# Performance work log

Measured on AMD Instinct MI355X. Metric: run time of the kernel, lower is better.

## Reference

```python
import jax, jax.numpy as jnp
import numpy as np

EXPERT_CAPACITY = 320
RMS_EPS = 1e-6


def setup_inputs() -> dict:
    key = jax.random.key(0)
    k1, k2, k3, k4 = jax.random.split(key, 4)
    B, S, D, E, F = 8, 2048, 1024, 8, 2048
    data = jax.random.normal(k1, (B, S, D), dtype=jnp.float32)
    gate_w = jax.random.normal(k2, (D, E), dtype=jnp.float32) * 0.02
    w1 = jax.random.normal(k3, (E, D, F), dtype=jnp.float32) * 0.02
    w2 = jax.random.normal(k4, (E, F, D), dtype=jnp.float32) * 0.02
    rms_w = jnp.ones((D,), dtype=jnp.float32)
    return {"data": data, "gate_w": gate_w, "w1": w1, "w2": w2, "rms_w": rms_w}


def reference(data, gate_w, w1, w2, rms_w):
    B, S, D = data.shape
    E = gate_w.shape[1]
    C = EXPERT_CAPACITY

    # norm_fn: RMSNorm
    var = jnp.mean(data * data, axis=-1, keepdims=True)
    norm = data * jax.lax.rsqrt(var + RMS_EPS) * rms_w  # [B,S,D]

    # route (fp32 gate, no jitter)
    logits = jnp.einsum('bsd,de->bse', norm, gate_w)  # [B,S,E]
    probs = jax.nn.softmax(logits, axis=-1)
    eidx = jnp.argmax(probs, axis=-1)  # [B,S] top-1 expert
    onehot = jax.nn.one_hot(eidx, E, dtype=jnp.int32)  # [B,S,E]
    priority = jnp.cumsum(onehot, axis=1)  # position within expert per batch row
    mask = onehot * (priority <= C)  # capacity-masked dispatch mask [B,S,E]

    pos = jnp.take_along_axis(priority, eidx[..., None], axis=2)[..., 0] - 1  # [B,S]
    kept = jnp.take_along_axis(mask, eidx[..., None], axis=2)[..., 0].astype(bool)
    pos_oob = jnp.where(kept, pos, C)  # OOB -> dropped on scatter

    # dispatch: scatter kept tokens into [B,E,C,D] buffers
    b_idx = jnp.arange(B)[:, None]  # broadcast over S
    buf = jnp.zeros((B, E, C, D), dtype=norm.dtype)
    buf = buf.at[b_idx, eidx, pos_oob].set(norm, mode='drop')

    # per-expert FFN with gelu_new (tanh approx)
    h = jax.nn.gelu(jnp.einsum('becd,edf->becf', buf, w1), approximate=True)
    out_buf = jnp.einsum('becf,efd->becd', h, w2)  # [B,E,C,D]

    # combine: gather expert output; dropped tokens keep norm_data (clone semantics)
    pos_c = jnp.clip(pos_oob, 0, C - 1)
    y = out_buf[b_idx, eidx, pos_c]  # [B,S,D]
    next_states = jnp.where(kept[..., None], y, norm)

    max_prob = jnp.max(probs, axis=-1, keepdims=True)
    hidden = max_prob * next_states
    final = data + hidden  # dropout rate 0

    expert_index_out = jnp.argmax(mask, axis=-1)  # matches torch argmax over masked one-hot
    return final, logits, expert_index_out
```

## Files before the change

### kernel.cpp

```cpp
#include <hip/hip_runtime.h>

typedef __attribute__((ext_vector_type(8))) __bf16 bf16x8;
typedef __attribute__((ext_vector_type(4))) float f32x4;

#define DEVI __device__ __forceinline__

DEVI unsigned short f2bf(float f) {
    unsigned u = __builtin_bit_cast(unsigned, f);
    u += 0x7fffu + ((u >> 16) & 1u);
    return (unsigned short)(u >> 16);
}
DEVI float bf2f(unsigned short h) {
    unsigned u = ((unsigned)h) << 16;
    return __builtin_bit_cast(float, u);
}
DEVI float gelu_tanh(float x) {
    float u = 0.7978845608028654f * (x + 0.044715f * x * x * x);
    float t = 1.0f - 2.0f / (1.0f + __expf(2.0f * u));
    return 0.5f * x * (1.0f + t);
}
DEVI void gload16(const void* g, void* l) {
    __builtin_amdgcn_global_load_lds((const __attribute__((address_space(1))) unsigned int*)g,
                                     (__attribute__((address_space(3))) unsigned int*)l,
                                     16, 0, 0);
}

#define BB 8
#define SS 2048
#define DD 1024
#define EE 8
#define FF 2048
#define CC 320
#define NTOK (BB * SS)
#define MPE (BB * CC)
#define NSLOT (EE * MPE)

__global__ __launch_bounds__(256) void k_rms_gate(
    const float* __restrict__ data, const float* __restrict__ gate_w,
    const float* __restrict__ rms_w, unsigned short* __restrict__ norm_bf,
    float* __restrict__ logits_out, float* __restrict__ maxprob, int* __restrict__ eidx_out,
    float* __restrict__ outF)
{
    const int token = blockIdx.x;
    const int t = threadIdx.x;
    const float4 v = ((const float4*)(data + (size_t)token * DD))[t];
    float ss = v.x * v.x + v.y * v.y + v.z * v.z + v.w * v.w;
#pragma unroll
    for (int o = 32; o; o >>= 1) ss += __shfl_down(ss, o, 64);
    __shared__ float sred[4];
    __shared__ float slog[8];
    __shared__ float sacc[4][8];
    __shared__ float smp;
    if ((t & 63) == 0) sred[t >> 6] = ss;
    __syncthreads();
    const float tot = sred[0] + sred[1] + sred[2] + sred[3];
    const float scale = rsqrtf(tot * (1.0f / 1024.0f) + 1e-6f);
    const float4 w = ((const float4*)rms_w)[t];
    float nn[4] = { v.x * scale * w.x, v.y * scale * w.y, v.z * scale * w.z, v.w * scale * w.w };
    ushort4 nb;
    nb.x = f2bf(nn[0]); nb.y = f2bf(nn[1]); nb.z = f2bf(nn[2]); nb.w = f2bf(nn[3]);
    ((ushort4*)(norm_bf + (size_t)token * DD))[t] = nb;

    float acc[8] = {0, 0, 0, 0, 0, 0, 0, 0};
    const float4* g = (const float4*)(gate_w + t * 32);
#pragma unroll
    for (int d = 0; d < 4; ++d) {
        float4 p = g[2 * d], q = g[2 * d + 1];
        acc[0] += nn[d] * p.x; acc[1] += nn[d] * p.y; acc[2] += nn[d] * p.z; acc[3] += nn[d] * p.w;
        acc[4] += nn[d] * q.x; acc[5] += nn[d] * q.y; acc[6] += nn[d] * q.z; acc[7] += nn[d] * q.w;
    }
#pragma unroll
    for (int e = 0; e < 8; ++e) {
#pragma unroll
        for (int o = 32; o; o >>= 1) acc[e] += __shfl_down(acc[e], o, 64);
    }
    if ((t & 63) == 0) {
#pragma unroll
        for (int e = 0; e < 8; ++e) sacc[t >> 6][e] = acc[e];
    }
    __syncthreads();
    if (t < 8) {
        float l = sacc[0][t] + sacc[1][t] + sacc[2][t] + sacc[3][t];
        logits_out[(size_t)token * 8 + t] = l;
        slog[t] = l;
    }
    __syncthreads();
    if (t == 0) {
        float m = slog[0]; int am = 0;
#pragma unroll
        for (int e = 1; e < 8; ++e) { if (slog[e] > m) { m = slog[e]; am = e; } }
        float s = 0.f;
#pragma unroll
        for (int e = 0; e < 8; ++e) s += __expf(slog[e] - m);
        const float mp = 1.0f / s;
        maxprob[token] = mp;
        smp = mp;
        eidx_out[token] = am;
    }
    __syncthreads();
    const float mp = smp;
    float4 o;
    o.x = v.x + mp * nn[0]; o.y = v.y + mp * nn[1];
    o.z = v.z + mp * nn[2]; o.w = v.w + mp * nn[3];
    ((float4*)(outF + (size_t)token * DD))[t] = o;
}

__global__ __launch_bounds__(256) void k_route(
    const int* __restrict__ eidx, float* __restrict__ idxf_out,
    int* __restrict__ slot_token, int* __restrict__ zp)
{
    const int b = blockIdx.x, t = threadIdx.x;
    if (b == 0) { zp[t] = 0; zp[t + 256] = 0; zp[t + 512] = 0; zp[t + 768] = 0; }
    for (int i = t; i < EE * CC; i += 256) {
        int e = i / CC, c = i % CC;
        slot_token[e * MPE + b * CC + c] = -1;
    }
    const int base = b * SS + t * 8;
    int e8[8];
#pragma unroll
    for (int j = 0; j < 8; ++j) e8[j] = eidx[base + j];
    int cnt[8] = {0, 0, 0, 0, 0, 0, 0, 0};
#pragma unroll
    for (int j = 0; j < 8; ++j) {
#pragma unroll
        for (int q = 0; q < 8; ++q) cnt[q] += (e8[j] == q);
    }
    __shared__ int sc[8][256];
#pragma unroll
    for (int q = 0; q < 8; ++q) sc[q][t] = cnt[q];
    __syncthreads();
    for (int off = 1; off < 256; off <<= 1) {
        int v[8];
#pragma unroll
        for (int q = 0; q < 8; ++q) v[q] = (t >= off) ? sc[q][t - off] : 0;
        __syncthreads();
#pragma unroll
        for (int q = 0; q < 8; ++q) sc[q][t] += v[q];
        __syncthreads();
    }
    int run[8];
#pragma unroll
    for (int q = 0; q < 8; ++q) run[q] = (t == 0) ? 0 : sc[q][t - 1];
#pragma unroll
    for (int j = 0; j < 8; ++j) {
        const int e = e8[j];
        const int tok = base + j;
        int pos = 0;
#pragma unroll
        for (int q = 0; q < 8; ++q) if (q == e) { pos = run[q]; run[q]++; }
        const bool kept = pos < CC;
        idxf_out[tok] = (float)(kept ? e : 0);
        if (kept) slot_token[e * MPE + b * CC + pos] = tok;
    }
}

__global__ __launch_bounds__(256) void k_transcvt3(
    const float* __restrict__ w1, const float* __restrict__ w2,
    unsigned short* __restrict__ w1T, unsigned short* __restrict__ w2T)
{
    __shared__ float tile[64][68];
    const int bid = blockIdx.x, t = threadIdx.x;
    const float* src; unsigned short* dst; int C, R, tr, tc;
    if (bid < 4096) {
        const int e = bid >> 9, rem = bid & 511;
        tr = rem >> 5; tc = rem & 31;
        src = w1 + (size_t)e * (DD * FF); dst = w1T + (size_t)e * (DD * FF);
        R = DD; C = FF;
    } else {
        const int b2 = bid - 4096;
        const int e = b2 >> 9, rem = b2 & 511;
        tr = rem >> 4; tc = rem & 15;
        src = w2 + (size_t)e * (DD * FF); dst = w2T + (size_t)e * (DD * FF);
        R = FF; C = DD;
    }
    const int r = t >> 2, c0 = (t & 3) << 4;
    const float4* sp = (const float4*)(src + (size_t)(tr * 64 + r) * C + tc * 64 + c0);
#pragma unroll
    for (int i = 0; i < 4; ++i) *(float4*)&tile[r][c0 + 4 * i] = sp[i];
    __syncthreads();
    const int oc = t >> 2, i0 = (t & 3) << 4;
    union { unsigned short us[16]; int4 q[2]; } u;
#pragma unroll
    for (int i = 0; i < 16; ++i) u.us[i] = f2bf(tile[i0 + i][oc]);
    unsigned short* dp = dst + (size_t)(tc * 64 + oc) * R + tr * 64 + i0;
    *(int4*)dp = u.q[0];
    *(int4*)(dp + 8) = u.q[1];
}

#define LD_A(buf, h) { _Pragma("unroll") for (int mp_ = 0; mp_ < 4; ++mp_) { \
    const int lr_ = mp_ * 16 + rr; \
    _Pragma("unroll") for (int ks_ = 0; ks_ < 2; ++ks_) \
      ar_[mp_][ks_] = *(const bf16x8*)(sm + (buf) * 65536 + (h) * 16384 + wm * 8192 + lr_ * 128 + ((ks_ * 64 + g * 16) ^ (((lr_ >> 2) & 1) << 5))); } }

#define LD_B(buf, h, reg) { _Pragma("unroll") for (int np_ = 0; np_ < 2; ++np_) { \
    const int lr_ = np_ * 16 + rr; \
    _Pragma("unroll") for (int ks_ = 0; ks_ < 2; ++ks_) \
      reg[np_][ks_] = *(const bf16x8*)(sm + (buf) * 65536 + 32768 + (h) * 16384 + wn * 4096 + lr_ * 128 + ((ks_ * 64 + g * 16) ^ (((lr_ >> 2) & 1) << 5))); } }

#define MM(qa, qb, reg) { _Pragma("unroll") for (int ks_ = 0; ks_ < 2; ++ks_) \
    _Pragma("unroll") for (int mp_ = 0; mp_ < 4; ++mp_) \
    _Pragma("unroll") for (int np_ = 0; np_ < 2; ++np_) \
      acc[(qa) * 4 + mp_][(qb) * 2 + np_] = __builtin_amdgcn_mfma_f32_16x16x32_bf16(ar_[mp_][ks_], reg[np_][ks_], acc[(qa) * 4 + mp_][(qb) * 2 + np_], 0, 0, 0); }

#define ST_A(buf, h, kt) { \
    gload16(srcA[h][0] + (kt) * 64, sm + (buf) * 65536 + (h) * 16384 + tid * 16); \
    gload16(srcA[h][1] + (kt) * 64, sm + (buf) * 65536 + (h) * 16384 + 8192 + tid * 16); }
#define ST_B(buf, h, kt) { \
    gload16(srcB[h][0] + (kt) * 64, sm + (buf) * 65536 + 32768 + (h) * 16384 + tid * 16); \
    gload16(srcB[h][1] + (kt) * 64, sm + (buf) * 65536 + 32768 + (h) * 16384 + 8192 + tid * 16); }

#define PH_TOP  __builtin_amdgcn_s_barrier(); \
                asm volatile("s_waitcnt lgkmcnt(0)" ::: "memory"); \
                __builtin_amdgcn_s_setprio(1)
#define PH_END  __builtin_amdgcn_s_setprio(0); __builtin_amdgcn_s_barrier()
#define PH_END_VM4 __builtin_amdgcn_s_setprio(0); \
                asm volatile("s_waitcnt vmcnt(4)" ::: "memory"); __builtin_amdgcn_s_barrier()
#define PH_END_VM0 __builtin_amdgcn_s_setprio(0); \
                asm volatile("s_waitcnt vmcnt(0)" ::: "memory"); __builtin_amdgcn_s_barrier()

template <int MODE, int K, int NT_N>
__global__ __launch_bounds__(512) void k_gemm8(
    const unsigned short* __restrict__ Ap, const unsigned short* __restrict__ Bt,
    unsigned short* __restrict__ H, const int* __restrict__ slot_token,
    const float* __restrict__ maxprob, const float* __restrict__ data,
    float* __restrict__ outF, const unsigned short* __restrict__ zp)
{
    __shared__ __align__(16) unsigned char sm[131072];
    const int bid = blockIdx.x;
    const int e = bid & 7;
    const int inner = bid >> 3;
    const int tm = inner / NT_N, tn = inner % NT_N;
    const int tid = threadIdx.x;
    const int L = tid & 63;
    const int wm = tid >> 8;
    const int wn = (tid >> 6) & 3;
    const int rr = L & 15, g = L >> 4;
    const int slot0 = e * MPE + tm * 256;
    const int N = NT_N * 256;

    const unsigned short* srcA[2][2];
    const unsigned short* srcB[2][2];
#pragma unroll
    for (int h = 0; h < 2; ++h)
#pragma unroll
      for (int p = 0; p < 2; ++p) {
        const int o = p * 8192 + tid * 16;
        const int lo = o ^ (((o >> 9) & 1) << 5);
        const int cb = lo & 127;
        const int arr = (lo >> 7) & 63;
        const int arow = p * 128 + h * 64 + arr;
        if (MODE == 0) {
            const int tok = slot_token[slot0 + arow];
            srcA[h][p] = (tok < 0 ? zp : Ap + (size_t)tok * (size_t)K) + (cb >> 1);
        } else {
            srcA[h][p] = Ap + (size_t)(slot0 + arow) * (size_t)K + (cb >> 1);
        }
        const int bwn = o >> 12;
        const int brr = (lo >> 7) & 31;
        const int nrow = tn * 256 + bwn * 64 + h * 32 + brr;
        srcB[h][p] = Bt + ((size_t)e * N + nrow) * (size_t)K + (cb >> 1);
    }

    f32x4 acc[8][4];
#pragma unroll
    for (int m = 0; m < 8; ++m)
#pragma unroll
      for (int n = 0; n < 4; ++n) acc[m][n] = 0.f;
    bf16x8 ar_[4][2], br0_[2][2], br1_[2][2];

    ST_A(0, 0, 0); ST_B(0, 0, 0); ST_A(0, 1, 0); ST_B(0, 1, 0);
    ST_A(1, 0, 1); ST_B(1, 1, 1);
    asm volatile("s_waitcnt vmcnt(4)" ::: "memory");
    __builtin_amdgcn_s_barrier();

    const int NT = K / 64;
    const int NITER = NT / 2;
    for (int it = 0; it < NITER - 1; ++it) {
        const int t1 = 2 * it + 1;
        LD_A(0, 0); LD_B(0, 0, br0_); ST_A(1, 1, t1);
        PH_TOP; MM(0, 0, br0_); PH_END;
        LD_B(0, 1, br1_); ST_B(1, 0, t1);
        PH_TOP; MM(0, 1, br1_); PH_END;
        LD_A(0, 1); ST_A(0, 0, t1 + 1);
        PH_TOP; MM(1, 1, br1_); PH_END;
        ST_B(0, 1, t1 + 1);
        PH_TOP; MM(1, 0, br0_); PH_END_VM4;
        LD_A(1, 0); LD_B(1, 0, br0_); ST_A(0, 1, t1 + 1);
        PH_TOP; MM(0, 0, br0_); PH_END;
        LD_B(1, 1, br1_); ST_B(0, 0, t1 + 1);
        PH_TOP; MM(0, 1, br1_); PH_END;
        LD_A(1, 1); ST_A(1, 0, t1 + 2);
        PH_TOP; MM(1, 1, br1_); PH_END;
        ST_B(1, 1, t1 + 2);
        PH_TOP; MM(1, 0, br0_); PH_END_VM4;
    }
    {
        LD_A(0, 0); LD_B(0, 0, br0_); ST_A(1, 1, NT - 1);
        PH_TOP; MM(0, 0, br0_); PH_END;
        LD_B(0, 1, br1_); ST_B(1, 0, NT - 1);
        PH_TOP; MM(0, 1, br1_); PH_END;
        LD_A(0, 1);
        PH_TOP; MM(1, 1, br1_); PH_END;
        PH_TOP; MM(1, 0, br0_); PH_END_VM0;
        LD_A(1, 0); LD_B(1, 0, br0_);
        PH_TOP; MM(0, 0, br0_); PH_END;
        LD_B(1, 1, br1_);
        PH_TOP; MM(0, 1, br1_); PH_END;
        LD_A(1, 1);
        PH_TOP; MM(1, 1, br1_); PH_END;
        PH_TOP; MM(1, 0, br0_); PH_END;
    }

    unsigned short* lo16 = (unsigned short*)sm;
#pragma unroll
    for (int hb = 0; hb < 2; ++hb) {
        if (wm == hb) {
#pragma unroll
            for (int m = 0; m < 8; ++m)
#pragma unroll
              for (int n = 0; n < 4; ++n) {
                f32x4 a = acc[m][n];
#pragma unroll
                for (int j = 0; j < 4; ++j) {
                    float x = a[j];
                    if (MODE == 0) x = gelu_tanh(x);
                    lo16[(m * 16 + g * 4 + j) * 260 + wn * 64 + n * 16 + rr] = f2bf(x);
                }
              }
        }
        __syncthreads();
#pragma unroll
        for (int rd = 0; rd < 8; ++rd) {
            const int idx = rd * 512 + tid;
            const int row = idx >> 5, c8 = (idx & 31) << 3;
            if (MODE == 0) {
                int4 v = *(const int4*)(lo16 + row * 260 + c8);
                *(int4*)(H + (size_t)(slot0 + hb * 128 + row) * FF + (size_t)tn * 256 + c8) = v;
            } else {
                const int tok = slot_token[slot0 + hb * 128 + row];
                if (tok >= 0) {
                    const float mp = maxprob[tok];
                    int4 yv = *(const int4*)(lo16 + row * 260 + c8);
                    const unsigned short* yy = (const unsigned short*)&yv;
                    const size_t go = (size_t)tok * DD + (size_t)tn * 256 + c8;
                    float4 d0 = *(const float4*)(data + go);
                    float4 d1 = *(const float4*)(data + go + 4);
                    float4 o0, o1;
                    o0.x = d0.x + mp * bf2f(yy[0]); o0.y = d0.y + mp * bf2f(yy[1]);
                    o0.z = d0.z + mp * bf2f(yy[2]); o0.w = d0.w + mp * bf2f(yy[3]);
                    o1.x = d1.x + mp * bf2f(yy[4]); o1.y = d1.y + mp * bf2f(yy[5]);
                    o1.z = d1.z + mp * bf2f(yy[6]); o1.w = d1.w + mp * bf2f(yy[7]);
                    *(float4*)(outF + go) = o0;
                    *(float4*)(outF + go + 4) = o1;
                }
            }
        }
        __syncthreads();
    }
}

extern "C" void kernel_launch(void* const* d_in, const int* in_sizes, int n_in,
                              void* d_out, int out_size, void* d_ws, size_t ws_size,
                              hipStream_t stream)
{
    (void)in_sizes; (void)n_in; (void)out_size; (void)ws_size;
    const float* data   = (const float*)d_in[0];
    const float* gate_w = (const float*)d_in[1];
    const float* w1     = (const float*)d_in[2];
    const float* w2     = (const float*)d_in[3];
    const float* rms_w  = (const float*)d_in[4];

    float* outF   = (float*)d_out;
    float* logits = outF + (size_t)NTOK * DD;
    float* idxf   = logits + (size_t)NTOK * EE;

    char* ws = (char*)d_ws;
    const size_t SZ_NORM = (size_t)NTOK * DD * 2;
    const size_t SZ_W1T  = (size_t)EE * DD * FF * 2;
    const size_t SZ_W2T  = SZ_W1T;
    const size_t SZ_H    = (size_t)NSLOT * FF * 2;
    unsigned short* norm_bf = (unsigned short*)(ws);
    unsigned short* w1T     = (unsigned short*)(ws + SZ_NORM);
    unsigned short* w2T     = (unsigned short*)(ws + SZ_NORM + SZ_W1T);
    unsigned short* Hbuf    = (unsigned short*)(ws + SZ_NORM + SZ_W1T + SZ_W2T);
    char* small             = ws + SZ_NORM + SZ_W1T + SZ_W2T + SZ_H;
    int*   slot_token = (int*)(small);
    int*   eidx       = (int*)(small + NSLOT * 4);
    float* maxprob    = (float*)(small + NSLOT * 4 + NTOK * 4);
    int*   zp         = (int*)(small + NSLOT * 4 + NTOK * 4 + NTOK * 4);

    k_rms_gate<<<NTOK, 256, 0, stream>>>(data, gate_w, rms_w, norm_bf, logits, maxprob, eidx, outF);
    k_route<<<BB, 256, 0, stream>>>(eidx, idxf, slot_token, zp);
    k_transcvt3<<<8192, 256, 0, stream>>>(w1, w2, w1T, w2T);
    k_gemm8<0, 1024, 8><<<640, 512, 0, stream>>>(norm_bf, w1T, Hbuf, slot_token,
                                                 nullptr, nullptr, nullptr, (const unsigned short*)zp);
    k_gemm8<1, 2048, 4><<<320, 512, 0, stream>>>(Hbuf, w2T, nullptr, slot_token,
                                                 maxprob, data, outF, nullptr);
}
```

Before: 565.4 us.

## Shrink expert GEMM tiles to 256x128 with new LDS swizzle and pipeline

```diff
diff --git a/kernel.cpp b/kernel.cpp
--- a/kernel.cpp
+++ b/kernel.cpp
@@ -187,128 +187,113 @@
     *(int4*)(dp + 8) = u.q[1];
 }
 
+#define AOFF(buf, h) ((buf) * 32768 + (h) * 16384)
+#define BOFF(buf, bh) (65536 + (buf) * 16384 + (bh) * 8192)
+
+#define ST_A(buf, h, kt) { \
+    gload16(srcA[h][0] + (kt) * 64, sm + AOFF(buf, h) + tid * 16); \
+    gload16(srcA[h][1] + (kt) * 64, sm + AOFF(buf, h) + 8192 + tid * 16); }
+#define ST_B(buf, bh, kt) { \
+    gload16(srcB[bh] + (kt) * 64, sm + BOFF(buf, bh) + tid * 16); }
+
 #define LD_A(buf, h) { _Pragma("unroll") for (int mp_ = 0; mp_ < 4; ++mp_) { \
-    const int lr_ = mp_ * 16 + rr; \
     _Pragma("unroll") for (int ks_ = 0; ks_ < 2; ++ks_) \
-      ar_[mp_][ks_] = *(const bf16x8*)(sm + (buf) * 65536 + (h) * 16384 + wm * 8192 + lr_ * 128 + ((ks_ * 64 + g * 16) ^ (((lr_ >> 2) & 1) << 5))); } }
-
-#define LD_B(buf, h, reg) { _Pragma("unroll") for (int np_ = 0; np_ < 2; ++np_) { \
-    const int lr_ = np_ * 16 + rr; \
+      ar_[mp_][ks_] = *(const bf16x8*)(sm + AOFF(buf, h) + wm * 8192 + (mp_ * 16 + rr) * 128 \
+                                       + ((ks_ * 64 + g * 16) ^ ((rr & 7) << 4))); } }
+#define LD_B(buf) { _Pragma("unroll") for (int qb_ = 0; qb_ < 2; ++qb_) { \
     _Pragma("unroll") for (int ks_ = 0; ks_ < 2; ++ks_) \
-      reg[np_][ks_] = *(const bf16x8*)(sm + (buf) * 65536 + 32768 + (h) * 16384 + wn * 4096 + lr_ * 128 + ((ks_ * 64 + g * 16) ^ (((lr_ >> 2) & 1) << 5))); } }
-
-#define MM(qa, qb, reg) { _Pragma("unroll") for (int ks_ = 0; ks_ < 2; ++ks_) \
+      br_[qb_][ks_] = *(const bf16x8*)(sm + BOFF(buf, qb_) + wn * 2048 + rr * 128 \
+                                       + ((ks_ * 64 + g * 16) ^ ((rr & 7) << 4))); } }
+
+#define MM(qa) { _Pragma("unroll") for (int ks_ = 0; ks_ < 2; ++ks_) \
     _Pragma("unroll") for (int mp_ = 0; mp_ < 4; ++mp_) \
-    _Pragma("unroll") for (int np_ = 0; np_ < 2; ++np_) \
-      acc[(qa) * 4 + mp_][(qb) * 2 + np_] = __builtin_amdgcn_mfma_f32_16x16x32_bf16(ar_[mp_][ks_], reg[np_][ks_], acc[(qa) * 4 + mp_][(qb) * 2 + np_], 0, 0, 0); }
-
-#define ST_A(buf, h, kt) { \
-    gload16(srcA[h][0] + (kt) * 64, sm + (buf) * 65536 + (h) * 16384 + tid * 16); \
-    gload16(srcA[h][1] + (kt) * 64, sm + (buf) * 65536 + (h) * 16384 + 8192 + tid * 16); }
-#define ST_B(buf, h, kt) { \
-    gload16(srcB[h][0] + (kt) * 64, sm + (buf) * 65536 + 32768 + (h) * 16384 + tid * 16); \
-    gload16(srcB[h][1] + (kt) * 64, sm + (buf) * 65536 + 32768 + (h) * 16384 + 8192 + tid * 16); }
+    _Pragma("unroll") for (int qb_ = 0; qb_ < 2; ++qb_) \
+      acc[(qa) * 4 + mp_][qb_] = __builtin_amdgcn_mfma_f32_16x16x32_bf16(ar_[mp_][ks_], br_[qb_][ks_], acc[(qa) * 4 + mp_][qb_], 0, 0, 0); }
 
 #define PH_TOP  __builtin_amdgcn_s_barrier(); \
                 asm volatile("s_waitcnt lgkmcnt(0)" ::: "memory"); \
                 __builtin_amdgcn_s_setprio(1)
 #define PH_END  __builtin_amdgcn_s_setprio(0); __builtin_amdgcn_s_barrier()
-#define PH_END_VM4 __builtin_amdgcn_s_setprio(0); \
-                asm volatile("s_waitcnt vmcnt(4)" ::: "memory"); __builtin_amdgcn_s_barrier()
+#define PH_END_VM3 __builtin_amdgcn_s_setprio(0); \
+                asm volatile("s_waitcnt vmcnt(3)" ::: "memory"); __builtin_amdgcn_s_barrier()
 #define PH_END_VM0 __builtin_amdgcn_s_setprio(0); \
                 asm volatile("s_waitcnt vmcnt(0)" ::: "memory"); __builtin_amdgcn_s_barrier()
 
-template <int MODE, int K, int NT_N>
-__global__ __launch_bounds__(512) void k_gemm8(
+template <int MODE, int K, int NN>
+__global__ __launch_bounds__(512) void k_gemm4(
     const unsigned short* __restrict__ Ap, const unsigned short* __restrict__ Bt,
     unsigned short* __restrict__ H, const int* __restrict__ slot_token,
     const float* __restrict__ maxprob, const float* __restrict__ data,
     float* __restrict__ outF, const unsigned short* __restrict__ zp)
 {
-    __shared__ __align__(16) unsigned char sm[131072];
+    __shared__ __align__(16) unsigned char sm[98304];
+    const int ntn = NN >> 7;
     const int bid = blockIdx.x;
     const int e = bid & 7;
     const int inner = bid >> 3;
-    const int tm = inner / NT_N, tn = inner % NT_N;
+    const int tm = inner / ntn, tn = inner % ntn;
     const int tid = threadIdx.x;
     const int L = tid & 63;
     const int wm = tid >> 8;
     const int wn = (tid >> 6) & 3;
     const int rr = L & 15, g = L >> 4;
     const int slot0 = e * MPE + tm * 256;
-    const int N = NT_N * 256;
 
     const unsigned short* srcA[2][2];
-    const unsigned short* srcB[2][2];
+    const unsigned short* srcB[2];
 #pragma unroll
     for (int h = 0; h < 2; ++h)
 #pragma unroll
       for (int p = 0; p < 2; ++p) {
         const int o = p * 8192 + tid * 16;
-        const int lo = o ^ (((o >> 9) & 1) << 5);
-        const int cb = lo & 127;
-        const int arr = (lo >> 7) & 63;
-        const int arow = p * 128 + h * 64 + arr;
+        const int cb = (o & 127) ^ (((o >> 7) & 7) << 4);
+        const int arow = p * 128 + h * 64 + ((o >> 7) & 63);
         if (MODE == 0) {
             const int tok = slot_token[slot0 + arow];
             srcA[h][p] = (tok < 0 ? zp : Ap + (size_t)tok * (size_t)K) + (cb >> 1);
         } else {
             srcA[h][p] = Ap + (size_t)(slot0 + arow) * (size_t)K + (cb >> 1);
         }
-        const int bwn = o >> 12;
-        const int brr = (lo >> 7) & 31;
-        const int nrow = tn * 256 + bwn * 64 + h * 32 + brr;
-        srcB[h][p] = Bt + ((size_t)e * N + nrow) * (size_t)K + (cb >> 1);
-    }
-
-    f32x4 acc[8][4];
-#pragma unroll
-    for (int m = 0; m < 8; ++m)
-#pragma unroll
-      for (int n = 0; n < 4; ++n) acc[m][n] = 0.f;
-    bf16x8 ar_[4][2], br0_[2][2], br1_[2][2];
-
-    ST_A(0, 0, 0); ST_B(0, 0, 0); ST_A(0, 1, 0); ST_B(0, 1, 0);
+      }
+#pragma unroll
+    for (int bh = 0; bh < 2; ++bh) {
+        const int o = tid * 16;
+        const int cb = (o & 127) ^ (((o >> 7) & 7) << 4);
+        const int nrow = tn * 128 + (o >> 11) * 32 + bh * 16 + ((o >> 7) & 15);
+        srcB[bh] = Bt + ((size_t)e * NN + nrow) * (size_t)K + (cb >> 1);
+    }
+
+    f32x4 acc[8][2];
+#pragma unroll
+    for (int m = 0; m < 8; ++m) { acc[m][0] = 0.f; acc[m][1] = 0.f; }
+    bf16x8 ar_[4][2], br_[2][2];
+
+    ST_A(0, 0, 0); ST_B(0, 1, 0); ST_A(0, 1, 0); ST_B(0, 0, 0);
     ST_A(1, 0, 1); ST_B(1, 1, 1);
-    asm volatile("s_waitcnt vmcnt(4)" ::: "memory");
+    asm volatile("s_waitcnt vmcnt(3)" ::: "memory");
     __builtin_amdgcn_s_barrier();
 
     const int NT = K / 64;
-    const int NITER = NT / 2;
-    for (int it = 0; it < NITER - 1; ++it) {
-        const int t1 = 2 * it + 1;
-        LD_A(0, 0); LD_B(0, 0, br0_); ST_A(1, 1, t1);
-        PH_TOP; MM(0, 0, br0_); PH_END;
-        LD_B(0, 1, br1_); ST_B(1, 0, t1);
-        PH_TOP; MM(0, 1, br1_); PH_END;
-        LD_A(0, 1); ST_A(0, 0, t1 + 1);
-        PH_TOP; MM(1, 1, br1_); PH_END;
-        ST_B(0, 1, t1 + 1);
-        PH_TOP; MM(1, 0, br0_); PH_END_VM4;
-        LD_A(1, 0); LD_B(1, 0, br0_); ST_A(0, 1, t1 + 1);
-        PH_TOP; MM(0, 0, br0_); PH_END;
-        LD_B(1, 1, br1_); ST_B(0, 0, t1 + 1);
-        PH_TOP; MM(0, 1, br1_); PH_END;
-        LD_A(1, 1); ST_A(1, 0, t1 + 2);
-        PH_TOP; MM(1, 1, br1_); PH_END;
-        ST_B(1, 1, t1 + 2);
-        PH_TOP; MM(1, 0, br0_); PH_END_VM4;
+    for (int it = 0; it < NT / 2 - 1; ++it) {
+        const int v = 2 * it + 1;
+        LD_A(0, 0); LD_B(0); ST_A(1, 1, v); ST_B(1, 0, v);
+        PH_TOP; MM(0); PH_END;
+        LD_A(0, 1); ST_A(0, 0, v + 1); ST_B(0, 1, v + 1);
+        PH_TOP; MM(1); PH_END_VM3;
+        LD_A(1, 0); LD_B(1); ST_A(0, 1, v + 1); ST_B(0, 0, v + 1);
+        PH_TOP; MM(0); PH_END;
+        LD_A(1, 1); ST_A(1, 0, v + 2); ST_B(1, 1, v + 2);
+        PH_TOP; MM(1); PH_END_VM3;
     }
     {
-        LD_A(0, 0); LD_B(0, 0, br0_); ST_A(1, 1, NT - 1);
-        PH_TOP; MM(0, 0, br0_); PH_END;
-        LD_B(0, 1, br1_); ST_B(1, 0, NT - 1);
-        PH_TOP; MM(0, 1, br1_); PH_END;
+        LD_A(0, 0); LD_B(0); ST_A(1, 1, NT - 1); ST_B(1, 0, NT - 1);
+        PH_TOP; MM(0); PH_END;
         LD_A(0, 1);
-        PH_TOP; MM(1, 1, br1_); PH_END;
-        PH_TOP; MM(1, 0, br0_); PH_END_VM0;
-        LD_A(1, 0); LD_B(1, 0, br0_);
-        PH_TOP; MM(0, 0, br0_); PH_END;
-        LD_B(1, 1, br1_);
-        PH_TOP; MM(0, 1, br1_); PH_END;
+        PH_TOP; MM(1); PH_END_VM0;
+        LD_A(1, 0); LD_B(1);
+        PH_TOP; MM(0); PH_END;
         LD_A(1, 1);
-        PH_TOP; MM(1, 1, br1_); PH_END;
-        PH_TOP; MM(1, 0, br0_); PH_END;
+        PH_TOP; MM(1); PH_END;
     }
 
     unsigned short* lo16 = (unsigned short*)sm;
@@ -318,31 +303,31 @@
 #pragma unroll
             for (int m = 0; m < 8; ++m)
 #pragma unroll
-              for (int n = 0; n < 4; ++n) {
-                f32x4 a = acc[m][n];
+              for (int qb = 0; qb < 2; ++qb) {
+                f32x4 a = acc[m][qb];
 #pragma unroll
                 for (int j = 0; j < 4; ++j) {
                     float x = a[j];
                     if (MODE == 0) x = gelu_tanh(x);
-                    lo16[(m * 16 + g * 4 + j) * 260 + wn * 64 + n * 16 + rr] = f2bf(x);
+                    lo16[(m * 16 + g * 4 + j) * 132 + wn * 32 + qb * 16 + rr] = f2bf(x);
                 }
               }
         }
         __syncthreads();
 #pragma unroll
-        for (int rd = 0; rd < 8; ++rd) {
+        for (int rd = 0; rd < 4; ++rd) {
             const int idx = rd * 512 + tid;
-            const int row = idx >> 5, c8 = (idx & 31) << 3;
+            const int row = idx >> 4, c8 = (idx & 15) << 3;
             if (MODE == 0) {
-                int4 v = *(const int4*)(lo16 + row * 260 + c8);
-                *(int4*)(H + (size_t)(slot0 + hb * 128 + row) * FF + (size_t)tn * 256 + c8) = v;
+                int4 v = *(const int4*)(lo16 + row * 132 + c8);
+                *(int4*)(H + (size_t)(slot0 + hb * 128 + row) * FF + (size_t)tn * 128 + c8) = v;
             } else {
                 const int tok = slot_token[slot0 + hb * 128 + row];
                 if (tok >= 0) {
                     const float mp = maxprob[tok];
-                    int4 yv = *(const int4*)(lo16 + row * 260 + c8);
+                    int4 yv = *(const int4*)(lo16 + row * 132 + c8);
                     const unsigned short* yy = (const unsigned short*)&yv;
-                    const size_t go = (size_t)tok * DD + (size_t)tn * 256 + c8;
+                    const size_t go = (size_t)tok * DD + (size_t)tn * 128 + c8;
                     float4 d0 = *(const float4*)(data + go);
                     float4 d1 = *(const float4*)(data + go + 4);
                     float4 o0, o1;
@@ -392,8 +377,8 @@
     k_rms_gate<<<NTOK, 256, 0, stream>>>(data, gate_w, rms_w, norm_bf, logits, maxprob, eidx, outF);
     k_route<<<BB, 256, 0, stream>>>(eidx, idxf, slot_token, zp);
     k_transcvt3<<<8192, 256, 0, stream>>>(w1, w2, w1T, w2T);
-    k_gemm8<0, 1024, 8><<<640, 512, 0, stream>>>(norm_bf, w1T, Hbuf, slot_token,
-                                                 nullptr, nullptr, nullptr, (const unsigned short*)zp);
-    k_gemm8<1, 2048, 4><<<320, 512, 0, stream>>>(Hbuf, w2T, nullptr, slot_token,
-                                                 maxprob, data, outF, nullptr);
-}
+    k_gemm4<0, 1024, 2048><<<1280, 512, 0, stream>>>(norm_bf, w1T, Hbuf, slot_token,
+                                                     nullptr, nullptr, nullptr, (const unsigned short*)zp);
+    k_gemm4<1, 2048, 1024><<<640, 512, 0, stream>>>(Hbuf, w2T, nullptr, slot_token,
+                                                    maxprob, data, outF, nullptr);
+}
```

Measured after the change: 531.3 us. 1.06x faster.

## Use one wave per token in RMS/gate and fix LDS swizzles

Applied to the files above, without the earlier changes.

```diff
diff --git a/kernel.cpp b/kernel.cpp
--- a/kernel.cpp
+++ b/kernel.cpp
@@ -41,68 +41,81 @@
     float* __restrict__ logits_out, float* __restrict__ maxprob, int* __restrict__ eidx_out,
     float* __restrict__ outF)
 {
-    const int token = blockIdx.x;
-    const int t = threadIdx.x;
-    const float4 v = ((const float4*)(data + (size_t)token * DD))[t];
-    float ss = v.x * v.x + v.y * v.y + v.z * v.z + v.w * v.w;
+    const int token = blockIdx.x * 4 + (threadIdx.x >> 6);
+    const int lane = threadIdx.x & 63;
+    const float* dp = data + (size_t)token * DD;
+
+    float4 v[4];
+#pragma unroll
+    for (int s = 0; s < 4; ++s) v[s] = *(const float4*)(dp + s * 256 + lane * 4);
+    float ss = 0.f;
+#pragma unroll
+    for (int s = 0; s < 4; ++s)
+        ss += v[s].x * v[s].x + v[s].y * v[s].y + v[s].z * v[s].z + v[s].w * v[s].w;
 #pragma unroll
     for (int o = 32; o; o >>= 1) ss += __shfl_down(ss, o, 64);
-    __shared__ float sred[4];
-    __shared__ float slog[8];
-    __shared__ float sacc[4][8];
-    __shared__ float smp;
-    if ((t & 63) == 0) sred[t >> 6] = ss;
-    __syncthreads();
-    const float tot = sred[0] + sred[1] + sred[2] + sred[3];
+    const float tot = __shfl(ss, 0, 64);
     const float scale = rsqrtf(tot * (1.0f / 1024.0f) + 1e-6f);
-    const float4 w = ((const float4*)rms_w)[t];
-    float nn[4] = { v.x * scale * w.x, v.y * scale * w.y, v.z * scale * w.z, v.w * scale * w.w };
-    ushort4 nb;
-    nb.x = f2bf(nn[0]); nb.y = f2bf(nn[1]); nb.z = f2bf(nn[2]); nb.w = f2bf(nn[3]);
-    ((ushort4*)(norm_bf + (size_t)token * DD))[t] = nb;
+
+    float nn[16];
+#pragma unroll
+    for (int s = 0; s < 4; ++s) {
+        const float4 w = *(const float4*)(rms_w + s * 256 + lane * 4);
+        nn[s * 4 + 0] = v[s].x * scale * w.x;
+        nn[s * 4 + 1] = v[s].y * scale * w.y;
+        nn[s * 4 + 2] = v[s].z * scale * w.z;
+        nn[s * 4 + 3] = v[s].w * scale * w.w;
+        ushort4 nb;
+        nb.x = f2bf(nn[s * 4 + 0]); nb.y = f2bf(nn[s * 4 + 1]);
+        nb.z = f2bf(nn[s * 4 + 2]); nb.w = f2bf(nn[s * 4 + 3]);
+        *(ushort4*)(norm_bf + (size_t)token * DD + s * 256 + lane * 4) = nb;
+    }
 
     float acc[8] = {0, 0, 0, 0, 0, 0, 0, 0};
-    const float4* g = (const float4*)(gate_w + t * 32);
-#pragma unroll
-    for (int d = 0; d < 4; ++d) {
-        float4 p = g[2 * d], q = g[2 * d + 1];
-        acc[0] += nn[d] * p.x; acc[1] += nn[d] * p.y; acc[2] += nn[d] * p.z; acc[3] += nn[d] * p.w;
-        acc[4] += nn[d] * q.x; acc[5] += nn[d] * q.y; acc[6] += nn[d] * q.z; acc[7] += nn[d] * q.w;
-    }
+#pragma unroll
+    for (int s = 0; s < 4; ++s)
+#pragma unroll
+      for (int j = 0; j < 4; ++j) {
+        const float4* g = (const float4*)(gate_w + (size_t)(s * 256 + lane * 4 + j) * 8);
+        const float4 p = g[0], q = g[1];
+        const float x = nn[s * 4 + j];
+        acc[0] += x * p.x; acc[1] += x * p.y; acc[2] += x * p.z; acc[3] += x * p.w;
+        acc[4] += x * q.x; acc[5] += x * q.y; acc[6] += x * q.z; acc[7] += x * q.w;
+      }
 #pragma unroll
     for (int e = 0; e < 8; ++e) {
 #pragma unroll
         for (int o = 32; o; o >>= 1) acc[e] += __shfl_down(acc[e], o, 64);
     }
-    if ((t & 63) == 0) {
-#pragma unroll
-        for (int e = 0; e < 8; ++e) sacc[t >> 6][e] = acc[e];
-    }
-    __syncthreads();
-    if (t < 8) {
-        float l = sacc[0][t] + sacc[1][t] + sacc[2][t] + sacc[3][t];
-        logits_out[(size_t)token * 8 + t] = l;
-        slog[t] = l;
-    }
-    __syncthreads();
-    if (t == 0) {
-        float m = slog[0]; int am = 0;
-#pragma unroll
-        for (int e = 1; e < 8; ++e) { if (slog[e] > m) { m = slog[e]; am = e; } }
+
+    float mp = 0.f;
+    if (lane == 0) {
+        float m = acc[0]; int am = 0;
+#pragma unroll
+        for (int e = 1; e < 8; ++e) { if (acc[e] > m) { m = acc[e]; am = e; } }
         float s = 0.f;
 #pragma unroll
-        for (int e = 0; e < 8; ++e) s += __expf(slog[e] - m);
-        const float mp = 1.0f / s;
+        for (int e = 0; e < 8; ++e) s += __expf(acc[e] - m);
+        mp = 1.0f / s;
         maxprob[token] = mp;
-        smp = mp;
         eidx_out[token] = am;
     }
-    __syncthreads();
-    const float mp = smp;
-    float4 o;
-    o.x = v.x + mp * nn[0]; o.y = v.y + mp * nn[1];
-    o.z = v.z + mp * nn[2]; o.w = v.w + mp * nn[3];
-    ((float4*)(outF + (size_t)token * DD))[t] = o;
+    mp = __shfl(mp, 0, 64);
+#pragma unroll
+    for (int e = 0; e < 8; ++e) {
+        const float l = __shfl(acc[e], 0, 64);
+        if (lane == e) logits_out[(size_t)token * 8 + e] = l;
+    }
+
+#pragma unroll
+    for (int s = 0; s < 4; ++s) {
+        float4 o;
+        o.x = v[s].x + mp * nn[s * 4 + 0];
+        o.y = v[s].y + mp * nn[s * 4 + 1];
+        o.z = v[s].z + mp * nn[s * 4 + 2];
+        o.w = v[s].w + mp * nn[s * 4 + 3];
+        *(float4*)(outF + (size_t)token * DD + s * 256 + lane * 4) = o;
+    }
 }
 
 __global__ __launch_bounds__(256) void k_route(
@@ -158,7 +171,7 @@
     const float* __restrict__ w1, const float* __restrict__ w2,
     unsigned short* __restrict__ w1T, unsigned short* __restrict__ w2T)
 {
-    __shared__ float tile[64][68];
+    __shared__ float tile[64][65];
     const int bid = blockIdx.x, t = threadIdx.x;
     const float* src; unsigned short* dst; int C, R, tr, tc;
     if (bid < 4096) {
@@ -190,12 +203,12 @@
 #define LD_A(buf, h) { _Pragma("unroll") for (int mp_ = 0; mp_ < 4; ++mp_) { \
     const int lr_ = mp_ * 16 + rr; \
     _Pragma("unroll") for (int ks_ = 0; ks_ < 2; ++ks_) \
-      ar_[mp_][ks_] = *(const bf16x8*)(sm + (buf) * 65536 + (h) * 16384 + wm * 8192 + lr_ * 128 + ((ks_ * 64 + g * 16) ^ (((lr_ >> 2) & 1) << 5))); } }
+      ar_[mp_][ks_] = *(const bf16x8*)(sm + (buf) * 65536 + (h) * 16384 + wm * 8192 + lr_ * 128 + ((ks_ * 64 + g * 16) ^ ((lr_ & 7) << 4))); } }
 
 #define LD_B(buf, h, reg) { _Pragma("unroll") for (int np_ = 0; np_ < 2; ++np_) { \
     const int lr_ = np_ * 16 + rr; \
     _Pragma("unroll") for (int ks_ = 0; ks_ < 2; ++ks_) \
-      reg[np_][ks_] = *(const bf16x8*)(sm + (buf) * 65536 + 32768 + (h) * 16384 + wn * 4096 + lr_ * 128 + ((ks_ * 64 + g * 16) ^ (((lr_ >> 2) & 1) << 5))); } }
+      reg[np_][ks_] = *(const bf16x8*)(sm + (buf) * 65536 + 32768 + (h) * 16384 + wn * 4096 + lr_ * 128 + ((ks_ * 64 + g * 16) ^ ((lr_ & 7) << 4))); } }
 
 #define MM(qa, qb, reg) { _Pragma("unroll") for (int ks_ = 0; ks_ < 2; ++ks_) \
     _Pragma("unroll") for (int mp_ = 0; mp_ < 4; ++mp_) \
@@ -245,9 +258,8 @@
 #pragma unroll
       for (int p = 0; p < 2; ++p) {
         const int o = p * 8192 + tid * 16;
-        const int lo = o ^ (((o >> 9) & 1) << 5);
-        const int cb = lo & 127;
-        const int arr = (lo >> 7) & 63;
+        const int cb = (o & 127) ^ (((o >> 7) & 7) << 4);
+        const int arr = (o >> 7) & 63;
         const int arow = p * 128 + h * 64 + arr;
         if (MODE == 0) {
             const int tok = slot_token[slot0 + arow];
@@ -256,7 +268,7 @@
             srcA[h][p] = Ap + (size_t)(slot0 + arow) * (size_t)K + (cb >> 1);
         }
         const int bwn = o >> 12;
-        const int brr = (lo >> 7) & 31;
+        const int brr = (o >> 7) & 31;
         const int nrow = tn * 256 + bwn * 64 + h * 32 + brr;
         srcB[h][p] = Bt + ((size_t)e * N + nrow) * (size_t)K + (cb >> 1);
     }
@@ -389,7 +401,7 @@
     float* maxprob    = (float*)(small + NSLOT * 4 + NTOK * 4);
     int*   zp         = (int*)(small + NSLOT * 4 + NTOK * 4 + NTOK * 4);
 
-    k_rms_gate<<<NTOK, 256, 0, stream>>>(data, gate_w, rms_w, norm_bf, logits, maxprob, eidx, outF);
+    k_rms_gate<<<NTOK / 4, 256, 0, stream>>>(data, gate_w, rms_w, norm_bf, logits, maxprob, eidx, outF);
     k_route<<<BB, 256, 0, stream>>>(eidx, idxf, slot_token, zp);
     k_transcvt3<<<8192, 256, 0, stream>>>(w1, w2, w1T, w2T);
     k_gemm8<0, 1024, 8><<<640, 512, 0, stream>>>(norm_bf, w1T, Hbuf, slot_token,
```

Result: faster. 542.6 us (-4.0%).
